# Kernel optimization log

Measured on AMD Instinct MI355X. Metric: run time of the kernel, lower is better.

Reference implementation:

```python
import jax, jax.numpy as jnp
import numpy as np

DIM = 256
N_EMBED = 1024
COMMITMENT_COST = 0.25


def setup_inputs() -> dict:
    key = jax.random.key(0)
    k1, k2 = jax.random.split(key)
    z = jax.random.normal(k1, (16, DIM, 64, 64), dtype=jnp.float32)
    lim = 1.0 / (2 * N_EMBED)
    embed_w = jax.random.uniform(k2, (N_EMBED, DIM), dtype=jnp.float32,
                                 minval=-lim, maxval=lim)
    return {"z": z, "embed_w": embed_w}


def reference(z, embed_w):
    # z: [B, C, H, W] -> [B, H, W, C]
    zp = jnp.transpose(z, (0, 2, 3, 1))
    B, H, W, C = zp.shape
    zf = zp.reshape(-1, C)  # [N, dim]
    # Squared euclidean distances to each codebook entry: [N, n_embed]
    d = (jnp.sum(zf * zf, axis=1, keepdims=True)
         + jnp.sum(embed_w * embed_w, axis=1)
         - 2.0 * jnp.matmul(zf, embed_w.T))
    idx = jnp.argmin(d, axis=1)  # [N]
    # Codebook lookup (equivalent to one-hot @ embed_w)
    z_q = embed_w[idx].reshape(zp.shape)  # [B, H, W, C]
    # VQ loss: codebook + commitment terms
    sg = jax.lax.stop_gradient
    loss = (jnp.mean((sg(z_q) - zp) ** 2)
            + COMMITMENT_COST * jnp.mean((z_q - sg(zp)) ** 2))
    # Straight-through estimator
    z_q_st = zp + sg(z_q - zp)
    # Perplexity from code usage histogram
    n = zf.shape[0]
    counts = jax.ops.segment_sum(jnp.ones((n,), jnp.float32), idx,
                                 num_segments=N_EMBED)
    e_mean = counts / n
    perplexity = jnp.exp(-jnp.sum(e_mean * jnp.log(e_mean + 1e-10)))
    z_q_out = jnp.transpose(z_q_st, (0, 3, 1, 2))  # back to [B, C, H, W]
    return loss, z_q_out, idx[:, None], perplexity
```

## Files before the change

kernel.cpp:

```cpp
#include <hip/hip_runtime.h>

#define BATCH 16
#define CDIM  256
#define HDIM  64
#define WDIM  64
#define NQ    65536
#define NE    1024
#define BM    32
#define KB    8
#define SECW  512

#define ZQ_OFF   1
#define IDX_OFF  16777217
#define PERP_OFF 16842753

#define WS_EE_OFF    0
#define WS_HIST_OFF  4096
#define WS_LOSS_OFF  8192
#define WS_WT_OFF    16384

__device__ __forceinline__ float pw128_sq(const float* __restrict__ p) {
    float r[8];
#pragma unroll
    for (int j = 0; j < 8; j++) r[j] = __fmul_rn(p[j], p[j]);
#pragma unroll
    for (int i = 8; i < 128; i += 8) {
#pragma unroll
        for (int j = 0; j < 8; j++) r[j] = __fadd_rn(r[j], __fmul_rn(p[i + j], p[i + j]));
    }
    return __fadd_rn(__fadd_rn(__fadd_rn(r[0], r[1]), __fadd_rn(r[2], r[3])),
                     __fadd_rn(__fadd_rn(r[4], r[5]), __fadd_rn(r[6], r[7])));
}

__global__ void vq_prep(const float* __restrict__ W, float* __restrict__ ee,
                        int* __restrict__ hist, double* __restrict__ loss_part) {
    int t = blockIdx.x * 256 + threadIdx.x;
    hist[t] = 0;
    if (t < 256) loss_part[t] = 0.0;
    const float* p = W + (size_t)t * CDIM;
    ee[t] = __fadd_rn(pw128_sq(p), pw128_sq(p + 128));
}

__global__ void vq_transpose(const float* __restrict__ W, float* __restrict__ WT) {
    __shared__ float T[64][65];
    const int e0 = (blockIdx.x & 15) * 64;
    const int k0 = (blockIdx.x >> 4) * 64;
    const int r  = threadIdx.x >> 4;
    const int c4 = threadIdx.x & 15;
#pragma unroll
    for (int s = 0; s < 4; s++) {
        float4 v = *(const float4*)(W + (size_t)(e0 + s * 16 + r) * CDIM + k0 + c4 * 4);
        T[s * 16 + r][c4 * 4 + 0] = v.x;
        T[s * 16 + r][c4 * 4 + 1] = v.y;
        T[s * 16 + r][c4 * 4 + 2] = v.z;
        T[s * 16 + r][c4 * 4 + 3] = v.w;
    }
    __syncthreads();
#pragma unroll
    for (int s = 0; s < 4; s++) {
        float4 o;
        o.x = T[c4 * 4 + 0][s * 16 + r];
        o.y = T[c4 * 4 + 1][s * 16 + r];
        o.z = T[c4 * 4 + 2][s * 16 + r];
        o.w = T[c4 * 4 + 3][s * 16 + r];
        *(float4*)(WT + (size_t)(k0 + s * 16 + r) * NE + e0 + c4 * 4) = o;
    }
}

__global__ __launch_bounds__(256, 2)
void vq_argmin(const float* __restrict__ z, const float* __restrict__ WT,
               const float* __restrict__ ee, float* __restrict__ out_idx,
               int* __restrict__ hist) {
    __shared__ __align__(16) float S[8192];
    __shared__ float zz_s[BM];
    __shared__ float tmp2[64];
    __shared__ float pD[BM][8];
    __shared__ int   pI[BM][8];

    float (*A)[BM]        = (float (*)[BM])S;
    float (*Bs)[KB][SECW] = (float (*)[KB][SECW])S;
    float (*redD)[64]     = (float (*)[64])S;
    int   (*redI)[64]     = (int   (*)[64])(S + 2048);

    const int t    = threadIdx.x;
    const int lane = t & 63;
    const int wv   = t >> 6;
    const int n0   = blockIdx.x * BM;
    const int b    = n0 >> 12;
    const int h    = (n0 >> 6) & 63;
    const int w0   = n0 & 63;

    const float* zb = z + (size_t)b * (CDIM * HDIM * WDIM) + (size_t)h * WDIM + w0;
#pragma unroll
    for (int v = 0; v < 8; v++) {
        int idx4 = v * 256 + t;
        int c  = idx4 >> 3;
        int w4 = idx4 & 7;
        *(float4*)(&A[c][w4 * 4]) = *(const float4*)(zb + (size_t)c * (HDIM * WDIM) + w4 * 4);
    }
    __syncthreads();

    if (t < 64) {
        int q = t >> 1, base = (t & 1) * 128;
        float r[8];
#pragma unroll
        for (int j = 0; j < 8; j++) { float x = A[base + j][q]; r[j] = __fmul_rn(x, x); }
        for (int i = 8; i < 128; i += 8) {
#pragma unroll
            for (int j = 0; j < 8; j++) { float x = A[base + i + j][q]; r[j] = __fadd_rn(r[j], __fmul_rn(x, x)); }
        }
        tmp2[t] = __fadd_rn(__fadd_rn(__fadd_rn(r[0], r[1]), __fadd_rn(r[2], r[3])),
                            __fadd_rn(__fadd_rn(r[4], r[5]), __fadd_rn(r[6], r[7])));
    }
    __syncthreads();
    if (t < BM) zz_s[t] = __fadd_rn(tmp2[2 * t], tmp2[2 * t + 1]);

    const int tx  = t & 63;
    const int q0  = wv * 8;
    const int q0u = __builtin_amdgcn_readfirstlane(q0);
    const float* aG = zb + q0u;

    auto stage = [&](int ssec, int skc, int nb) {
#pragma unroll
        for (int v = 0; v < 4; v++) {
            const int s_  = v * 4 + wv;
            const int r_  = s_ >> 1;
            const int hf_ = s_ & 1;
            const float* g_ = WT + (size_t)(skc * KB + r_) * NE + ssec * SECW + hf_ * 256 + lane * 4;
            __builtin_amdgcn_global_load_lds(
                (const __attribute__((address_space(1))) void*)g_,
                (__attribute__((address_space(3))) void*)(&Bs[nb][r_][hf_ * 256]),
                16, 0, 0);
        }
    };

    float bestD[8]; int bestI[8];
#pragma unroll
    for (int i = 0; i < 8; i++) { bestD[i] = 3.0e38f; bestI[i] = 0; }

    stage(0, 0, 0);
    __syncthreads();

    for (int sec = 0; sec < 2; sec++) {
        float acc[8][8];
#pragma unroll
        for (int i = 0; i < 8; i++)
#pragma unroll
            for (int j = 0; j < 8; j++) acc[i][j] = 0.0f;

        for (int kc = 0; kc < 32; kc++) {
            const int cur = kc & 1;
            {
                int nkc = kc + 1, nsec = sec;
                if (nkc == 32) { nkc = 0; nsec++; }
                if (nsec < 2) stage(nsec, nkc, cur ^ 1);
            }
            const int kb = kc * KB;
#pragma unroll
            for (int k2 = 0; k2 < KB; k2++) {
                const float4 b4a = *(const float4*)(&Bs[cur][k2][tx * 4]);
                const float4 b4b = *(const float4*)(&Bs[cur][k2][256 + tx * 4]);
                const float* ar = aG + (size_t)(kb + k2) * 4096;
                float av[8];
#pragma unroll
                for (int i = 0; i < 8; i++) av[i] = ar[i];
                float bv[8] = {b4a.x, b4a.y, b4a.z, b4a.w, b4b.x, b4b.y, b4b.z, b4b.w};
#pragma unroll
                for (int i = 0; i < 8; i++)
#pragma unroll
                    for (int j = 0; j < 8; j++)
                        acc[i][j] = __fmaf_rn(av[i], bv[j], acc[i][j]);
            }
            __syncthreads();
        }

        const int e0a = sec * SECW + tx * 4;
        const int e0b = e0a + 256;
        float4 eeA = *(const float4*)(ee + e0a);
        float4 eeB = *(const float4*)(ee + e0b);
        float eva[4] = {eeA.x, eeA.y, eeA.z, eeA.w};
        float evb[4] = {eeB.x, eeB.y, eeB.z, eeB.w};
#pragma unroll
        for (int i = 0; i < 8; i++) {
            float zzq = zz_s[q0 + i];
#pragma unroll
            for (int j = 0; j < 4; j++) {
                float s = __fadd_rn(zzq, eva[j]);
                float d = __fsub_rn(s, __fadd_rn(acc[i][j], acc[i][j]));
                if (d < bestD[i]) { bestD[i] = d; bestI[i] = e0a + j; }
            }
#pragma unroll
            for (int j = 0; j < 4; j++) {
                float s = __fadd_rn(zzq, evb[j]);
                float d = __fsub_rn(s, __fadd_rn(acc[i][4 + j], acc[i][4 + j]));
                if (d < bestD[i]) { bestD[i] = d; bestI[i] = e0b + j; }
            }
        }
    }

    __syncthreads();
#pragma unroll
    for (int i = 0; i < 8; i++) { redD[q0 + i][tx] = bestD[i]; redI[q0 + i][tx] = bestI[i]; }
    __syncthreads();
    {
        int q = t >> 3, s8 = t & 7;
        float bd = redD[q][s8 * 8]; int bi = redI[q][s8 * 8];
#pragma unroll
        for (int u = 1; u < 8; u++) {
            float d2 = redD[q][s8 * 8 + u]; int i2 = redI[q][s8 * 8 + u];
            if (d2 < bd || (d2 == bd && i2 < bi)) { bd = d2; bi = i2; }
        }
        pD[q][s8] = bd; pI[q][s8] = bi;
    }
    __syncthreads();
    if (t < BM) {
        float bd = pD[t][0]; int bi = pI[t][0];
#pragma unroll
        for (int u = 1; u < 8; u++) {
            float d2 = pD[t][u]; int i2 = pI[t][u];
            if (d2 < bd || (d2 == bd && i2 < bi)) { bd = d2; bi = i2; }
        }
        out_idx[n0 + t] = (float)bi;
        atomicAdd(&hist[bi], 1);
    }
}

__global__ void vq_gather(const float* __restrict__ z, const float* __restrict__ W,
                          const float* __restrict__ idxf, float* __restrict__ zq_out,
                          double* __restrict__ loss_part) {
    const int gid = blockIdx.x * 256 + threadIdx.x;
    const int w4 = gid & 15;
    const int r  = gid >> 4;
    const int h  = r & 63;
    const int c  = (r >> 6) & 255;
    const int b  = r >> 14;
    const size_t off = (((size_t)(b * CDIM + c) * HDIM + h) * WDIM) + w4 * 4;
    const float4 zp = *(const float4*)(z + off);
    const int n = b * 4096 + h * 64 + w4 * 4;

    float zpv[4] = {zp.x, zp.y, zp.z, zp.w};
    float ov[4];
    double ls = 0.0;
#pragma unroll
    for (int l = 0; l < 4; l++) {
        int idx = (int)idxf[n + l];
        float zq = W[(size_t)idx * CDIM + c];
        float t1 = __fsub_rn(zq, zpv[l]);
        ov[l] = __fadd_rn(zpv[l], t1);
        ls += (double)t1 * (double)t1;
    }
    float4 o = {ov[0], ov[1], ov[2], ov[3]};
    *(float4*)(zq_out + off) = o;

#pragma unroll
    for (int s = 32; s > 0; s >>= 1) ls += __shfl_down(ls, s, 64);
    __shared__ double wsum[4];
    if ((threadIdx.x & 63) == 0) wsum[threadIdx.x >> 6] = ls;
    __syncthreads();
    if (threadIdx.x == 0) {
        double v = wsum[0] + wsum[1] + wsum[2] + wsum[3];
        atomicAdd(&loss_part[blockIdx.x & 255], v);
    }
}

__global__ void vq_final(const double* __restrict__ loss_part, const int* __restrict__ hist,
                         float* __restrict__ d_out) {
    __shared__ double s1[256], s2[256];
    const int t = threadIdx.x;
    double v = loss_part[t];
    double pv = 0.0;
#pragma unroll
    for (int j = 0; j < 4; j++) {
        int cnt = hist[t * 4 + j];
        double em = (double)cnt / 65536.0;
        pv += em * log(em + 1e-10);
    }
    s1[t] = v; s2[t] = pv;
    __syncthreads();
    for (int st = 128; st > 0; st >>= 1) {
        if (t < st) { s1[t] += s1[t + st]; s2[t] += s2[t + st]; }
        __syncthreads();
    }
    if (t == 0) {
        float m = (float)(s1[0] / 16777216.0);
        d_out[0] = 1.25f * m;
        d_out[PERP_OFF] = (float)exp(-s2[0]);
    }
}

extern "C" void kernel_launch(void* const* d_in, const int* in_sizes, int n_in,
                              void* d_out, int out_size, void* d_ws, size_t ws_size,
                              hipStream_t stream) {
    const float* z = (const float*)d_in[0];
    const float* W = (const float*)d_in[1];
    float* out = (float*)d_out;

    float*  ee        = (float*)((char*)d_ws + WS_EE_OFF);
    int*    hist      = (int*)((char*)d_ws + WS_HIST_OFF);
    double* loss_part = (double*)((char*)d_ws + WS_LOSS_OFF);
    float*  WT        = (float*)((char*)d_ws + WS_WT_OFF);

    vq_prep<<<4, 256, 0, stream>>>(W, ee, hist, loss_part);
    vq_transpose<<<64, 256, 0, stream>>>(W, WT);
    vq_argmin<<<NQ / BM, 256, 0, stream>>>(z, WT, ee, out + IDX_OFF, hist);
    vq_gather<<<(NQ * CDIM / 4) / 256, 256, 0, stream>>>(z, W, out + IDX_OFF, out + ZQ_OFF, loss_part);
    vq_final<<<1, 256, 0, stream>>>(loss_part, hist, out);
}
```

Baseline: 550.9 us.

## Software-pipeline z loads into registers and spill running argmin to LDS

Replaces the per-k scalar global loads of z with float4 vector loads, double-buffered in registers two k-steps ahead, so global latency overlaps the FMA work. Running best distances and indices are kept in a dedicated LDS region between the two codebook sections instead of in registers. This cuts register pressure to make room for the prefetch buffers. The cost is larger shared memory (48KB), which may limit occupancy with launch bounds of 2 blocks, plus wrap-around loads at the end of the loop.

```diff
diff --git a/kernel.cpp b/kernel.cpp
--- a/kernel.cpp
+++ b/kernel.cpp
@@ -71,7 +71,7 @@
 void vq_argmin(const float* __restrict__ z, const float* __restrict__ WT,
                const float* __restrict__ ee, float* __restrict__ out_idx,
                int* __restrict__ hist) {
-    __shared__ __align__(16) float S[8192];
+    __shared__ __align__(16) float S[12288];
     __shared__ float zz_s[BM];
     __shared__ float tmp2[64];
     __shared__ float pD[BM][8];
@@ -79,8 +79,8 @@
 
     float (*A)[BM]        = (float (*)[BM])S;
     float (*Bs)[KB][SECW] = (float (*)[KB][SECW])S;
-    float (*redD)[64]     = (float (*)[64])S;
-    int   (*redI)[64]     = (int   (*)[64])(S + 2048);
+    float (*redD)[64]     = (float (*)[64])(S + 8192);
+    int   (*redI)[64]     = (int   (*)[64])(S + 10240);
 
     const int t    = threadIdx.x;
     const int lane = t & 63;
@@ -115,10 +115,9 @@
     __syncthreads();
     if (t < BM) zz_s[t] = __fadd_rn(tmp2[2 * t], tmp2[2 * t + 1]);
 
-    const int tx  = t & 63;
-    const int q0  = wv * 8;
-    const int q0u = __builtin_amdgcn_readfirstlane(q0);
-    const float* aG = zb + q0u;
+    const int tx = t & 63;
+    const int q0 = wv * 8;
+    const float* aq = zb + q0;
 
     auto stage = [&](int ssec, int skc, int nb) {
 #pragma unroll
@@ -134,11 +133,43 @@
         }
     };
 
-    float bestD[8]; int bestI[8];
-#pragma unroll
-    for (int i = 0; i < 8; i++) { bestD[i] = 3.0e38f; bestI[i] = 0; }
+#define LOADA2(K, X0, X1, X2, X3)                                   \
+    {                                                               \
+        const float* ap0_ = aq + (size_t)((K) & 255) * 4096;        \
+        const float* ap1_ = aq + (size_t)(((K) + 1) & 255) * 4096;  \
+        X0 = *(const float4*)ap0_;                                  \
+        X1 = *(const float4*)(ap0_ + 4);                            \
+        X2 = *(const float4*)ap1_;                                  \
+        X3 = *(const float4*)(ap1_ + 4);                            \
+    }
+
+#define COMPUTE2(CUR, K2, A0, A1, A2, A3)                                      \
+    {                                                                          \
+        const float4 ba0 = *(const float4*)(&Bs[CUR][K2][tx * 4]);             \
+        const float4 bb0 = *(const float4*)(&Bs[CUR][K2][256 + tx * 4]);       \
+        float avv[8] = {A0.x, A0.y, A0.z, A0.w, A1.x, A1.y, A1.z, A1.w};       \
+        float bvv[8] = {ba0.x, ba0.y, ba0.z, ba0.w, bb0.x, bb0.y, bb0.z, bb0.w};\
+        _Pragma("unroll")                                                      \
+        for (int i = 0; i < 8; i++)                                            \
+            _Pragma("unroll")                                                  \
+            for (int j = 0; j < 8; j++)                                        \
+                acc[i][j] = __fmaf_rn(avv[i], bvv[j], acc[i][j]);              \
+        const float4 ba1 = *(const float4*)(&Bs[CUR][(K2) + 1][tx * 4]);       \
+        const float4 bb1 = *(const float4*)(&Bs[CUR][(K2) + 1][256 + tx * 4]); \
+        float avw[8] = {A2.x, A2.y, A2.z, A2.w, A3.x, A3.y, A3.z, A3.w};       \
+        float bvw[8] = {ba1.x, ba1.y, ba1.z, ba1.w, bb1.x, bb1.y, bb1.z, bb1.w};\
+        _Pragma("unroll")                                                      \
+        for (int i = 0; i < 8; i++)                                            \
+            _Pragma("unroll")                                                  \
+            for (int j = 0; j < 8; j++)                                        \
+                acc[i][j] = __fmaf_rn(avw[i], bvw[j], acc[i][j]);              \
+    }
+
+    float4 pA0, pA1, pA2, pA3, nA0, nA1, nA2, nA3;
 
     stage(0, 0, 0);
+    LOADA2(0, pA0, pA1, pA2, pA3)
+    LOADA2(2, nA0, nA1, nA2, nA3)
     __syncthreads();
 
     for (int sec = 0; sec < 2; sec++) {
@@ -156,21 +187,14 @@
                 if (nsec < 2) stage(nsec, nkc, cur ^ 1);
             }
             const int kb = kc * KB;
-#pragma unroll
-            for (int k2 = 0; k2 < KB; k2++) {
-                const float4 b4a = *(const float4*)(&Bs[cur][k2][tx * 4]);
-                const float4 b4b = *(const float4*)(&Bs[cur][k2][256 + tx * 4]);
-                const float* ar = aG + (size_t)(kb + k2) * 4096;
-                float av[8];
-#pragma unroll
-                for (int i = 0; i < 8; i++) av[i] = ar[i];
-                float bv[8] = {b4a.x, b4a.y, b4a.z, b4a.w, b4b.x, b4b.y, b4b.z, b4b.w};
-#pragma unroll
-                for (int i = 0; i < 8; i++)
-#pragma unroll
-                    for (int j = 0; j < 8; j++)
-                        acc[i][j] = __fmaf_rn(av[i], bv[j], acc[i][j]);
-            }
+            COMPUTE2(cur, 0, pA0, pA1, pA2, pA3)
+            LOADA2(kb + 4, pA0, pA1, pA2, pA3)
+            COMPUTE2(cur, 2, nA0, nA1, nA2, nA3)
+            LOADA2(kb + 6, nA0, nA1, nA2, nA3)
+            COMPUTE2(cur, 4, pA0, pA1, pA2, pA3)
+            LOADA2(kb + 8, pA0, pA1, pA2, pA3)
+            COMPUTE2(cur, 6, nA0, nA1, nA2, nA3)
+            LOADA2(kb + 10, nA0, nA1, nA2, nA3)
             __syncthreads();
         }
 
@@ -182,25 +206,28 @@
         float evb[4] = {eeB.x, eeB.y, eeB.z, eeB.w};
 #pragma unroll
         for (int i = 0; i < 8; i++) {
-            float zzq = zz_s[q0 + i];
+            float bd; int bi;
+            if (sec == 0) { bd = 3.0e38f; bi = 0; }
+            else          { bd = redD[q0 + i][tx]; bi = redI[q0 + i][tx]; }
+            const float zzq = zz_s[q0 + i];
 #pragma unroll
             for (int j = 0; j < 4; j++) {
                 float s = __fadd_rn(zzq, eva[j]);
                 float d = __fsub_rn(s, __fadd_rn(acc[i][j], acc[i][j]));
-                if (d < bestD[i]) { bestD[i] = d; bestI[i] = e0a + j; }
+                if (d < bd) { bd = d; bi = e0a + j; }
             }
 #pragma unroll
             for (int j = 0; j < 4; j++) {
                 float s = __fadd_rn(zzq, evb[j]);
                 float d = __fsub_rn(s, __fadd_rn(acc[i][4 + j], acc[i][4 + j]));
-                if (d < bestD[i]) { bestD[i] = d; bestI[i] = e0b + j; }
+                if (d < bd) { bd = d; bi = e0b + j; }
             }
-        }
-    }
-
-    __syncthreads();
-#pragma unroll
-    for (int i = 0; i < 8; i++) { redD[q0 + i][tx] = bestD[i]; redI[q0 + i][tx] = bestI[i]; }
+            redD[q0 + i][tx] = bd; redI[q0 + i][tx] = bi;
+        }
+    }
+#undef COMPUTE2
+#undef LOADA2
+
     __syncthreads();
     {
         int q = t >> 3, s8 = t & 7;
```

Measured after the change: 735.3 us. 33.5% more time.

## Stage codebook rows in shared memory for coalesced gather and straight-through output

Applied to the files above, without the earlier changes.

The gather kernel now gives each block 32 consecutive spatial positions. It loads their selected codebook rows into a swizzled LDS tile with coalesced float4 reads. Each thread then walks 32 channels, reading z and writing the output with scalar accesses that are contiguous across w. This replaces the old scheme, where each thread did four scattered per-channel codebook loads, and it also drops the float4 store to the output buffer at offset 1, which is not 16-byte aligned. In exchange, z reads and output writes become scalar rather than vector accesses, and the kernel uses more LDS per block.

```diff
diff --git a/kernel.cpp b/kernel.cpp
--- a/kernel.cpp
+++ b/kernel.cpp
@@ -225,39 +225,55 @@
     }
 }
 
-__global__ void vq_gather(const float* __restrict__ z, const float* __restrict__ W,
-                          const float* __restrict__ idxf, float* __restrict__ zq_out,
-                          double* __restrict__ loss_part) {
-    const int gid = blockIdx.x * 256 + threadIdx.x;
-    const int w4 = gid & 15;
-    const int r  = gid >> 4;
-    const int h  = r & 63;
-    const int c  = (r >> 6) & 255;
-    const int b  = r >> 14;
-    const size_t off = (((size_t)(b * CDIM + c) * HDIM + h) * WDIM) + w4 * 4;
-    const float4 zp = *(const float4*)(z + off);
-    const int n = b * 4096 + h * 64 + w4 * 4;
-
-    float zpv[4] = {zp.x, zp.y, zp.z, zp.w};
-    float ov[4];
+__global__ __launch_bounds__(256, 2)
+void vq_gather(const float* __restrict__ z, const float* __restrict__ W,
+               const float* __restrict__ idxf, float* __restrict__ zq_out,
+               double* __restrict__ loss_part) {
+    __shared__ int    idx_s[32];
+    __shared__ float  zq_s[32][256];
+    __shared__ double wsum[4];
+
+    const int t    = threadIdx.x;
+    const int lane = t & 63;
+    const int wv   = t >> 6;
+    const int n0   = blockIdx.x * 32;
+    const int b    = n0 >> 12;
+    const int h    = (n0 >> 6) & 63;
+    const int w0   = n0 & 63;
+
+    if (t < 32) idx_s[t] = (int)idxf[n0 + t];
+    __syncthreads();
+
+#pragma unroll
+    for (int j = 0; j < 8; j++) {
+        const int q   = wv * 8 + j;
+        const int idx = idx_s[q];
+        float4 v = *(const float4*)(W + (size_t)idx * CDIM + lane * 4);
+        *(float4*)(&zq_s[q][(lane * 4) ^ ((q & 7) << 2)]) = v;
+    }
+    __syncthreads();
+
+    const int w  = t & 31;
+    const int cb = (t >> 5) * 32;
+    const int sw = (w & 7) << 2;
+    const size_t base = (size_t)b * (CDIM * HDIM * WDIM) + (size_t)h * WDIM + w0 + w;
     double ls = 0.0;
-#pragma unroll
-    for (int l = 0; l < 4; l++) {
-        int idx = (int)idxf[n + l];
-        float zq = W[(size_t)idx * CDIM + c];
-        float t1 = __fsub_rn(zq, zpv[l]);
-        ov[l] = __fadd_rn(zpv[l], t1);
+#pragma unroll 8
+    for (int cc = 0; cc < 32; cc++) {
+        const int c = cb + cc;
+        const float zq = zq_s[w][c ^ sw];
+        const size_t off = base + (size_t)c * (HDIM * WDIM);
+        const float zp = z[off];
+        const float t1 = __fsub_rn(zq, zp);
+        zq_out[off] = __fadd_rn(zp, t1);
         ls += (double)t1 * (double)t1;
     }
-    float4 o = {ov[0], ov[1], ov[2], ov[3]};
-    *(float4*)(zq_out + off) = o;
 
 #pragma unroll
     for (int s = 32; s > 0; s >>= 1) ls += __shfl_down(ls, s, 64);
-    __shared__ double wsum[4];
-    if ((threadIdx.x & 63) == 0) wsum[threadIdx.x >> 6] = ls;
-    __syncthreads();
-    if (threadIdx.x == 0) {
+    if (lane == 0) wsum[wv] = ls;
+    __syncthreads();
+    if (t == 0) {
         double v = wsum[0] + wsum[1] + wsum[2] + wsum[3];
         atomicAdd(&loss_part[blockIdx.x & 255], v);
     }
@@ -303,6 +319,6 @@
     vq_prep<<<4, 256, 0, stream>>>(W, ee, hist, loss_part);
     vq_transpose<<<64, 256, 0, stream>>>(W, WT);
     vq_argmin<<<NQ / BM, 256, 0, stream>>>(z, WT, ee, out + IDX_OFF, hist);
-    vq_gather<<<(NQ * CDIM / 4) / 256, 256, 0, stream>>>(z, W, out + IDX_OFF, out + ZQ_OFF, loss_part);
+    vq_gather<<<NQ / 32, 256, 0, stream>>>(z, W, out + IDX_OFF, out + ZQ_OFF, loss_part);
     vq_final<<<1, 256, 0, stream>>>(loss_part, hist, out);
 }
```

After: 514.6 us. 6.6% less time.
